# Kernel optimization log

Measured on AMD Instinct MI355X. Metric: run time of the kernel, lower is better.

## Reference

```python
import jax, jax.numpy as jnp
import numpy as np

FEAT = 1024
SUPPORT = 512
N = 4096


def setup_inputs() -> dict:
    key = jax.random.key(0)
    k1, k2, k3, k4, k5, k6 = jax.random.split(key, 6)
    s = 1.0 / np.sqrt(FEAT)
    f = jax.random.normal(k1, (N, FEAT), dtype=jnp.float32)
    G = jax.random.normal(k2, (SUPPORT, FEAT), dtype=jnp.float32)
    # PyTorch LSTMCell params: weight_ih [4*hidden, input], weight_hh [4*hidden, hidden]
    W_ih = jax.random.uniform(k3, (4 * FEAT, 2 * FEAT), minval=-s, maxval=s, dtype=jnp.float32)
    W_hh = jax.random.uniform(k4, (4 * FEAT, FEAT), minval=-s, maxval=s, dtype=jnp.float32)
    b_ih = jax.random.uniform(k5, (4 * FEAT,), minval=-s, maxval=s, dtype=jnp.float32)
    b_hh = jax.random.uniform(k6, (4 * FEAT,), minval=-s, maxval=s, dtype=jnp.float32)
    return {"f": f, "G": G, "W_ih": W_ih, "W_hh": W_hh, "b_ih": b_ih, "b_hh": b_hh, "n_ways": 20}


def _lstm_cell(x, h, c, W_ih, W_hh, b_ih, b_hh):
    # gates ordered i, f, g, o as in torch.nn.LSTMCell
    gates = x @ W_ih.T + b_ih + h @ W_hh.T + b_hh  # [N, 4*FEAT]
    i, fg, g, o = jnp.split(gates, 4, axis=1)
    i = jax.nn.sigmoid(i)
    fg = jax.nn.sigmoid(fg)
    g = jnp.tanh(g)
    o = jax.nn.sigmoid(o)
    c_new = fg * c + i * g
    h_new = o * jnp.tanh(c_new)
    return h_new, c_new


def reference(f, G, W_ih, W_hh, b_ih, b_hh, n_ways):
    h = f
    c = jnp.zeros_like(f)  # c_0 expanded, zeros (non-learned Variable)
    for _ in range(n_ways):
        logit_a = h @ G.T                      # [N, M]
        a = jax.nn.softmax(logit_a, axis=0)    # softmax over dim 0, as in original
        r = a @ G                              # [N, FEAT]
        x = jnp.concatenate((f, r), axis=1)    # [N, 2*FEAT]
        h, c = _lstm_cell(x, h, c, W_ih, W_hh, b_ih, b_hh)
        h = h + f
    return h
```

## Files before the change

### kernel.cpp

```cpp
#include <hip/hip_runtime.h>
#include <math.h>

#define NB    4096
#define FEAT  1024
#define MSUP  512
#define G4    4096
#define NWAYS 20

typedef _Float16 f16;
typedef f16 f16x8 __attribute__((ext_vector_type(8)));
typedef f16 f16x4 __attribute__((ext_vector_type(4)));
typedef float f32x4 __attribute__((ext_vector_type(4)));
typedef unsigned int u32;
#define GLOBAL_AS __attribute__((address_space(1)))
#define LDS_AS    __attribute__((address_space(3)))

__device__ __forceinline__ void load_lds16(const void* g, void* l) {
    __builtin_amdgcn_global_load_lds((const GLOBAL_AS u32*)g, (LDS_AS u32*)l, 16, 0, 0);
}

__device__ __forceinline__ float sigm(float x) { return 1.f / (1.f + __expf(-x)); }

template<int BM, int BN, int WROWS, int WCOLS, bool OUTF16, bool HASBIAS>
__global__ __launch_bounds__(256) void mfma_nt(
    void* __restrict__ Cv, int ldc,
    const f16* __restrict__ A1, int lda1, const f16* __restrict__ B1, int ldb1, int K1,
    const f16* __restrict__ A2, int lda2, const f16* __restrict__ B2, int ldb2, int K2,
    const f16* __restrict__ A3, int lda3, const f16* __restrict__ B3, int ldb3, int K3,
    const float* __restrict__ bias)
{
    constexpr int BK = 32;
    constexpr int WM = BM / WROWS, WN = BN / WCOLS;
    constexpr int FM = WM / 16,   FN = WN / 16;
    __shared__ f16 As[BM][BK];
    __shared__ f16 Bs[BN][BK];
    const int tid  = threadIdx.x;
    const int lane = tid & 63;
    const int wrow = (tid >> 6) % WROWS, wcol = (tid >> 6) / WROWS;
    const int bm = blockIdx.y * BM, bn = blockIdx.x * BN;
    const int lr = lane & 15, lq = lane >> 4;

    f32x4 acc[FM][FN] = {};

    #pragma unroll
    for (int pass = 0; pass < 3; ++pass) {
        const f16* A = pass == 0 ? A1 : (pass == 1 ? A2 : A3);
        const f16* B = pass == 0 ? B1 : (pass == 1 ? B2 : B3);
        const int lda = pass == 0 ? lda1 : (pass == 1 ? lda2 : lda3);
        const int ldb = pass == 0 ? ldb1 : (pass == 1 ? ldb2 : ldb3);
        const int K   = pass == 0 ? K1  : (pass == 1 ? K2  : K3);
        if (!A) break;
        #pragma unroll 1
        for (int k0 = 0; k0 < K; k0 += BK) {
            __syncthreads();
            #pragma unroll
            for (int t = 0; t < (BM * 4) / 256; ++t) {
                int c = t * 256 + tid;
                load_lds16(A + (size_t)(bm + (c >> 2)) * lda + k0 + (c & 3) * 8,
                           &As[0][0] + ((size_t)t * 256 + (tid & 192)) * 8);
            }
            #pragma unroll
            for (int t = 0; t < (BN * 4) / 256; ++t) {
                int c = t * 256 + tid;
                load_lds16(B + (size_t)(bn + (c >> 2)) * ldb + k0 + (c & 3) * 8,
                           &Bs[0][0] + ((size_t)t * 256 + (tid & 192)) * 8);
            }
            __syncthreads();
            f16x8 af[FM], bf[FN];
            #pragma unroll
            for (int i = 0; i < FM; ++i)
                af[i] = *(const f16x8*)&As[wrow * WM + i * 16 + lr][lq * 8];
            #pragma unroll
            for (int j = 0; j < FN; ++j)
                bf[j] = *(const f16x8*)&Bs[wcol * WN + j * 16 + lr][lq * 8];
            #pragma unroll
            for (int i = 0; i < FM; ++i)
                #pragma unroll
                for (int j = 0; j < FN; ++j)
                    acc[i][j] = __builtin_amdgcn_mfma_f32_16x16x32_f16(af[i], bf[j], acc[i][j], 0, 0, 0);
        }
    }

    #pragma unroll
    for (int i = 0; i < FM; ++i) {
        #pragma unroll
        for (int j = 0; j < FN; ++j) {
            const int col  = bn + wcol * WN + j * 16 + lr;
            const int row0 = bm + wrow * WM + i * 16 + lq * 4;
            float badd = HASBIAS ? bias[col] : 0.f;
            #pragma unroll
            for (int r = 0; r < 4; ++r) {
                size_t off = (size_t)(row0 + r) * ldc + col;
                float v = acc[i][j][r] + badd;
                if (OUTF16) ((f16*)Cv)[off] = (f16)v;
                else        ((float*)Cv)[off] = v;
            }
        }
    }
}

__global__ __launch_bounds__(512, 2) void gates_8p(
    const f16* __restrict__ a,
    const f16* __restrict__ h,
    const f16* __restrict__ Wcat,
    const f16* __restrict__ pre,
    const float* __restrict__ fin,
    float* __restrict__ cbuf,
    f16* __restrict__ hh,
    float* __restrict__ hout,
    int first, int writeH)
{
    extern __shared__ f16x8 smem8[];
    f16* smem = (f16*)smem8;
    const int tid  = threadIdx.x;
    const int lane = tid & 63;
    const int wid  = tid >> 6;
    const int wrow = wid >> 2, wcol = wid & 3;
    const int lr = lane & 15, lq = lane >> 4;

    const int bidr = blockIdx.y * 16 + blockIdx.x;
    const int wg   = (bidr & 7) * 32 + (bidr >> 3);
    const int bm = (wg >> 4) * 256;
    const int bn = (wg & 15) * 256;

    f32x4 acc[8][4] = {};

    auto stage = [&](const f16* src, int ld, int rb, int ko, f16* lbase, int l) {
        int c = l * 512 + tid;
        int r = c >> 3;
        int x = (c & 7) ^ (r & 7);
        load_lds16(src + (size_t)(rb + r) * ld + ko + (x << 3),
                   lbase + ((size_t)(l * 512 + (tid & 448))) * 8);
    };
    #define RDF(BUF, RB, KK) \
        (*(const f16x8*)((BUF) + ((size_t)((RB) + lr) << 6) + ((((KK) << 2 | lq) ^ (lr & 7)) << 3)))
    #define BAR()  asm volatile("s_barrier" ::: "memory")
    #define SBAR() __builtin_amdgcn_sched_barrier(0)

    #pragma unroll
    for (int l = 0; l < 4; ++l) {
        stage(Wcat, 2048, bn, 0, smem + 16384, l);
        stage(a,    MSUP, bm, 0, smem,         l);
    }
    asm volatile("s_waitcnt vmcnt(0)" ::: "memory");
    BAR();

    #pragma unroll 1
    for (int t = 0; t < 32; ++t) {
        f16* Ab = smem + (t & 1) * 32768;
        f16* Bb = Ab + 16384;
        f16* An = smem + ((t + 1) & 1) * 32768;
        f16* Bn = An + 16384;
        const int k1 = (t + 1) * 64;
        const f16* As2 = a; int lda2 = MSUP, ko2 = k1;
        if (k1 >= 1024)     { As2 = h; lda2 = FEAT; ko2 = k1 - 1024; }
        else if (k1 >= 512) { ko2 = k1 - 512; }
        const bool st = (t < 31);

        f16x8 af[4][2], bf[2][2], bg[2][2];

        #pragma unroll
        for (int i = 0; i < 4; ++i)
            #pragma unroll
            for (int kk = 0; kk < 2; ++kk)
                af[i][kk] = RDF(Ab, wrow * 128 + i * 16, kk);
        #pragma unroll
        for (int j = 0; j < 2; ++j)
            #pragma unroll
            for (int kk = 0; kk < 2; ++kk)
                bf[j][kk] = RDF(Bb, wcol * 64 + j * 16, kk);
        if (st) {
            stage(Wcat, 2048, bn, k1, Bn, 0);
            stage(Wcat, 2048, bn, k1, Bn, 1);
            stage(Wcat, 2048, bn, k1, Bn, 2);
        }
        BAR(); SBAR();
        __builtin_amdgcn_s_setprio(1);
        #pragma unroll
        for (int kk = 0; kk < 2; ++kk)
            #pragma unroll
            for (int i = 0; i < 4; ++i)
                #pragma unroll
                for (int j = 0; j < 2; ++j)
                    acc[i][j] = __builtin_amdgcn_mfma_f32_16x16x32_f16(af[i][kk], bf[j][kk], acc[i][j], 0, 0, 0);
        __builtin_amdgcn_s_setprio(0);
        BAR();

        #pragma unroll
        for (int j = 0; j < 2; ++j)
            #pragma unroll
            for (int kk = 0; kk < 2; ++kk)
                bg[j][kk] = RDF(Bb, wcol * 64 + (j + 2) * 16, kk);
        if (st) {
            stage(Wcat, 2048, bn, k1, Bn, 3);
            stage(As2, lda2, bm, ko2, An, 0);
            stage(As2, lda2, bm, ko2, An, 2);
        }
        BAR(); SBAR();
        __builtin_amdgcn_s_setprio(1);
        #pragma unroll
        for (int kk = 0; kk < 2; ++kk)
            #pragma unroll
            for (int i = 0; i < 4; ++i)
                #pragma unroll
                for (int j = 0; j < 2; ++j)
                    acc[i][j + 2] = __builtin_amdgcn_mfma_f32_16x16x32_f16(af[i][kk], bg[j][kk], acc[i][j + 2], 0, 0, 0);
        __builtin_amdgcn_s_setprio(0);
        if (st) asm volatile("s_waitcnt vmcnt(6)" ::: "memory");
        else    asm volatile("s_waitcnt vmcnt(0)" ::: "memory");
        BAR();

        #pragma unroll
        for (int i = 0; i < 4; ++i)
            #pragma unroll
            for (int kk = 0; kk < 2; ++kk)
                af[i][kk] = RDF(Ab, wrow * 128 + (i + 4) * 16, kk);
        if (st) {
            stage(As2, lda2, bm, ko2, An, 1);
            stage(As2, lda2, bm, ko2, An, 3);
        }
        BAR(); SBAR();
        __builtin_amdgcn_s_setprio(1);
        #pragma unroll
        for (int kk = 0; kk < 2; ++kk)
            #pragma unroll
            for (int i = 0; i < 4; ++i)
                #pragma unroll
                for (int j = 0; j < 2; ++j)
                    acc[i + 4][j + 2] = __builtin_amdgcn_mfma_f32_16x16x32_f16(af[i][kk], bg[j][kk], acc[i + 4][j + 2], 0, 0, 0);
        __builtin_amdgcn_s_setprio(0);
        BAR();

        #pragma unroll
        for (int j = 0; j < 2; ++j)
            #pragma unroll
            for (int kk = 0; kk < 2; ++kk)
                bf[j][kk] = RDF(Bb, wcol * 64 + j * 16, kk);
        BAR(); SBAR();
        __builtin_amdgcn_s_setprio(1);
        #pragma unroll
        for (int kk = 0; kk < 2; ++kk)
            #pragma unroll
            for (int i = 0; i < 4; ++i)
                #pragma unroll
                for (int j = 0; j < 2; ++j)
                    acc[i + 4][j] = __builtin_amdgcn_mfma_f32_16x16x32_f16(af[i][kk], bf[j][kk], acc[i + 4][j], 0, 0, 0);
        __builtin_amdgcn_s_setprio(0);
        if (st) asm volatile("s_waitcnt vmcnt(2)" ::: "memory");
        BAR();
    }
    #undef RDF

    const int q  = lane & 3;
    const int fk = (lane >> 2) & 3;
    #pragma unroll
    for (int i = 0; i < 8; ++i) {
        #pragma unroll
        for (int j = 0; j < 4; ++j) {
            const int cb   = bn + wcol * 64 + j * 16;
            const int row0 = bm + wrow * 128 + i * 16 + lq * 4;
            float x[4];
            #pragma unroll
            for (int r = 0; r < 4; ++r) x[r] = acc[i][j][r];
            float g4[4];
            #pragma unroll
            for (int k = 0; k < 4; ++k) {
                int srcq = (q + k) & 3;
                int src  = (lane & ~3) | srcq;
                g4[srcq] = __shfl(x[(q - k + 4) & 3], src, 64);
            }
            const int row  = row0 + q;
            const int feat = (cb >> 2) + fk;
            f16x4 p = *(const f16x4*)(pre + (size_t)row * G4 + cb + 4 * fk);
            const float i_ = sigm(g4[0] + (float)p[0]);
            const float f_ = sigm(g4[1] + (float)p[1]);
            const float g_ = tanhf(g4[2] + (float)p[2]);
            const float o_ = sigm(g4[3] + (float)p[3]);
            const size_t cid = ((size_t)(blockIdx.y * gridDim.x + blockIdx.x) * 32
                                + i * 4 + j) * 512 + tid;
            float cold = first ? 0.f : cbuf[cid];
            float cn = i_ * g_ + f_ * cold;
            cbuf[cid] = cn;
            float hn = o_ * tanhf(cn) + fin[(size_t)row * FEAT + feat];
            hh[(size_t)row * FEAT + feat] = (f16)hn;
            if (writeH) hout[(size_t)row * FEAT + feat] = hn;
        }
    }
}

__global__ __launch_bounds__(256) void softmax_rows_kernel(
    const float* __restrict__ X, f16* __restrict__ Y)
{
    const int row = blockIdx.x;
    const float* x = X + (size_t)row * NB;
    f16* y = Y + (size_t)row * NB;
    const int tid = threadIdx.x;
    float v[16];
    float mx = -1e30f;
    #pragma unroll
    for (int i = 0; i < 16; ++i) { v[i] = x[tid + (i << 8)]; mx = fmaxf(mx, v[i]); }
    #pragma unroll
    for (int off = 32; off > 0; off >>= 1) mx = fmaxf(mx, __shfl_down(mx, off));
    __shared__ float sm[4];
    if ((tid & 63) == 0) sm[tid >> 6] = mx;
    __syncthreads();
    mx = fmaxf(fmaxf(sm[0], sm[1]), fmaxf(sm[2], sm[3]));
    float s = 0.f;
    #pragma unroll
    for (int i = 0; i < 16; ++i) { v[i] = __expf(v[i] - mx); s += v[i]; }
    #pragma unroll
    for (int off = 32; off > 0; off >>= 1) s += __shfl_down(s, off);
    __shared__ float ss[4];
    if ((tid & 63) == 0) ss[tid >> 6] = s;
    __syncthreads();
    s = ss[0] + ss[1] + ss[2] + ss[3];
    const float inv = 1.f / s;
    #pragma unroll
    for (int i = 0; i < 16; ++i) y[tid + (i << 8)] = (f16)(v[i] * inv);
}

__global__ __launch_bounds__(256) void transpose_f16_kernel(
    const f16* __restrict__ in, f16* __restrict__ out, int R, int C)
{
    __shared__ f16 t[64][65];
    const int r0 = blockIdx.y * 64, c0 = blockIdx.x * 64;
    const int lr = threadIdx.x & 63, lw = threadIdx.x >> 6;
    #pragma unroll
    for (int i = 0; i < 16; ++i) {
        int rr = lw * 16 + i;
        t[rr][lr] = in[(size_t)(r0 + rr) * C + c0 + lr];
    }
    __syncthreads();
    #pragma unroll
    for (int i = 0; i < 16; ++i) {
        int cc = lw * 16 + i;
        out[(size_t)(c0 + cc) * R + r0 + lr] = t[lr][cc];
    }
}

__global__ __launch_bounds__(256) void cvt_f16_kernel(
    const float* __restrict__ in, f16* __restrict__ out, int n)
{
    int idx = (blockIdx.x * 256 + threadIdx.x) * 4;
    if (idx < n) {
        float4 v = *(const float4*)(in + idx);
        f16x4 o = {(f16)v.x, (f16)v.y, (f16)v.z, (f16)v.w};
        *(f16x4*)(out + idx) = o;
    }
}

__global__ __launch_bounds__(256) void cvt_perm_kernel(
    const float* __restrict__ in, f16* __restrict__ out, int ld_in, int ld_out, int col_off)
{
    int idx = (blockIdx.x * 256 + threadIdx.x) * 4;
    int j = idx / ld_in, k = idx % ld_in;
    int dst = 4 * (j & 1023) + (j >> 10);
    float4 v = *(const float4*)(in + idx);
    f16x4 o = {(f16)v.x, (f16)v.y, (f16)v.z, (f16)v.w};
    *(f16x4*)(out + (size_t)dst * ld_out + col_off + k) = o;
}

__global__ __launch_bounds__(256) void bias_perm_kernel(
    const float* __restrict__ bih, const float* __restrict__ bhh, float* __restrict__ out)
{
    int j = blockIdx.x * 256 + threadIdx.x;
    out[4 * (j & 1023) + (j >> 10)] = bih[j] + bhh[j];
}

__global__ __launch_bounds__(256) void split_wcat_kernel(
    const float* __restrict__ in, f16* __restrict__ out)
{
    int idx = (blockIdx.x * 256 + threadIdx.x) * 4;
    int g = idx >> 9, k = idx & 511;
    float4 v = *(const float4*)(in + idx);
    f16x4 hi = {(f16)v.x, (f16)v.y, (f16)v.z, (f16)v.w};
    f16x4 lo = {(f16)(v.x - (float)hi.x), (f16)(v.y - (float)hi.y),
                (f16)(v.z - (float)hi.z), (f16)(v.w - (float)hi.w)};
    *(f16x4*)(out + (size_t)g * 2048 + k) = hi;
    *(f16x4*)(out + (size_t)g * 2048 + 512 + k) = lo;
}

extern "C" void kernel_launch(void* const* d_in, const int* in_sizes, int n_in,
                              void* d_out, int out_size, void* d_ws, size_t ws_size,
                              hipStream_t stream) {
    const float* f   = (const float*)d_in[0];
    const float* G   = (const float*)d_in[1];
    const float* Wih = (const float*)d_in[2];
    const float* Whh = (const float*)d_in[3];
    const float* bih = (const float*)d_in[4];
    const float* bhh = (const float*)d_in[5];
    float* h = (float*)d_out;

    char* W = (char*)d_ws;
    f16*   pre_h   = (f16*)(W);
    float* aT      = (float*)(W + (size_t)(32 << 20));
    f16*   aTh     = (f16*)(W + (size_t)(40 << 20));
    f16*   a_h     = (f16*)(W + (size_t)(44 << 20));
    float* cbuf    = (float*)(W + (size_t)(48 << 20));
    f16*   h0      = (f16*)(W + (size_t)(64 << 20));
    f16*   hA      = (f16*)(W + (size_t)(72 << 20));
    f16*   hB      = (f16*)(W + (size_t)(80 << 20));
    f16*   Wih_h   = (f16*)(W + (size_t)(88 << 20));
    f16*   Wcat    = (f16*)(W + (size_t)(104 << 20));
    float* Wr32    = (float*)(W + (size_t)(120 << 20));
    f16*   G_h     = (f16*)(W + (size_t)(128 << 20));
    float* bias_p  = (float*)(W + (size_t)(129 << 20));

    const f16* NF = nullptr;
    const dim3 blk(256);

    hipFuncSetAttribute((const void*)gates_8p,
                        hipFuncAttributeMaxDynamicSharedMemorySize, 131072);

    cvt_f16_kernel<<<(NB * FEAT) / 1024, blk, 0, stream>>>(f, h0, NB * FEAT);
    cvt_perm_kernel<<<(G4 * 2 * FEAT) / 1024, blk, 0, stream>>>(Wih, Wih_h, 2 * FEAT, 2 * FEAT, 0);
    cvt_perm_kernel<<<(G4 * FEAT) / 1024, blk, 0, stream>>>(Whh, Wcat, FEAT, 2048, 1024);
    cvt_f16_kernel<<<(MSUP * FEAT) / 1024, blk, 0, stream>>>(G, G_h, MSUP * FEAT);
    bias_perm_kernel<<<G4 / 256, blk, 0, stream>>>(bih, bhh, bias_p);

    mfma_nt<128, 128, 2, 2, true, true><<<dim3(G4 / 128, NB / 128), blk, 0, stream>>>(
        pre_h, G4,
        h0, FEAT, Wih_h, 2 * FEAT, FEAT,
        NF, 0, NF, 0, 0, NF, 0, NF, 0, 0,
        bias_p);

    mfma_nt<128, 128, 2, 2, false, false><<<dim3(MSUP / 128, G4 / 128), blk, 0, stream>>>(
        Wr32, MSUP,
        Wih_h + FEAT, 2 * FEAT, G_h, FEAT, FEAT,
        NF, 0, NF, 0, 0, NF, 0, NF, 0, 0,
        nullptr);
    split_wcat_kernel<<<(G4 * MSUP) / 1024, blk, 0, stream>>>(Wr32, Wcat);

    const f16* hcur = h0;
    for (int it = 0; it < NWAYS; ++it) {
        mfma_nt<64, 64, 2, 2, false, false><<<dim3(NB / 64, MSUP / 64), blk, 0, stream>>>(
            aT, NB,
            G_h, FEAT, hcur, FEAT, FEAT,
            NF, 0, NF, 0, 0, NF, 0, NF, 0, 0,
            nullptr);

        softmax_rows_kernel<<<MSUP, blk, 0, stream>>>(aT, aTh);
        transpose_f16_kernel<<<dim3(NB / 64, MSUP / 64), blk, 0, stream>>>(aTh, a_h, MSUP, NB);

        f16* hnext = (it & 1) ? hB : hA;
        gates_8p<<<dim3(G4 / 256, NB / 256), 512, 131072, stream>>>(
            a_h, hcur, Wcat, pre_h, f, cbuf, hnext, h, it == 0, it == NWAYS - 1);
        hcur = hnext;
    }
}
```

Baseline: 2.436 ms.

## Restructure fused LSTM GEMM main loop with inline-asm LDS reads and prefetch

Rewrites the 256x256 fused LSTM gate GEMM main loop to issue LDS reads through inline-asm ds_read_b128 with precomputed swizzled base addresses and immediate offsets. The loop is unrolled by two so double-buffer addresses are constants. All eight global-to-LDS stages for the next tile are issued at once after a vmcnt wait, and the A/B fragments for the next tile are prefetched during the last MFMA block of the current tile. Fine-grained lgkmcnt waits replace full barriers between sub-blocks. This aims to cut address arithmetic and LDS-read latency stalls, at the cost of more registers and hand-managed waitcnt correctness.

```diff
diff --git a/kernel.cpp b/kernel.cpp
--- a/kernel.cpp
+++ b/kernel.cpp
@@ -20,6 +20,14 @@
 }
 
 __device__ __forceinline__ float sigm(float x) { return 1.f / (1.f + __expf(-x)); }
+
+#define RD(dst, base, OFF) \
+    asm volatile("ds_read_b128 %0, %1 offset:" OFF : "=v"(dst) : "v"(base))
+
+__device__ __forceinline__ f32x4 mfma16(f32x4 a, f32x4 b, f32x4 c) {
+    return __builtin_amdgcn_mfma_f32_16x16x32_f16(
+        __builtin_bit_cast(f16x8, a), __builtin_bit_cast(f16x8, b), c, 0, 0, 0);
+}
 
 template<int BM, int BN, int WROWS, int WCOLS, bool OUTF16, bool HASBIAS>
 __global__ __launch_bounds__(256) void mfma_nt(
@@ -125,56 +133,75 @@
 
     f32x4 acc[8][4] = {};
 
-    auto stage = [&](const f16* src, int ld, int rb, int ko, f16* lbase, int l) {
-        int c = l * 512 + tid;
-        int r = c >> 3;
-        int x = (c & 7) ^ (r & 7);
-        load_lds16(src + (size_t)(rb + r) * ld + ko + (x << 3),
-                   lbase + ((size_t)(l * 512 + (tid & 448))) * 8);
+    const int rr8 = tid >> 3;
+    const int xx8 = ((tid & 7) ^ (rr8 & 7)) << 3;
+    const int plA = rr8 * MSUP + xx8;
+    const int plH = rr8 * FEAT + xx8;
+    const int plW = rr8 * 2048 + xx8;
+    const int ldst = (tid & 448) * 8;
+
+    auto stageW = [&](int ko, f16* lbase, int l) {
+        load_lds16(Wcat + (size_t)(bn + l * 64) * 2048 + ko + plW,
+                   lbase + l * 4096 + ldst);
     };
-    #define RDF(BUF, RB, KK) \
-        (*(const f16x8*)((BUF) + ((size_t)((RB) + lr) << 6) + ((((KK) << 2 | lq) ^ (lr & 7)) << 3)))
-    #define BAR()  asm volatile("s_barrier" ::: "memory")
-    #define SBAR() __builtin_amdgcn_sched_barrier(0)
-
-    #pragma unroll
-    for (int l = 0; l < 4; ++l) {
-        stage(Wcat, 2048, bn, 0, smem + 16384, l);
-        stage(a,    MSUP, bm, 0, smem,         l);
-    }
-    asm volatile("s_waitcnt vmcnt(0)" ::: "memory");
+    auto stageA = [&](const f16* src, int ld, int pl, int ko, f16* lbase, int l) {
+        load_lds16(src + (size_t)(bm + l * 64) * ld + ko + pl,
+                   lbase + l * 4096 + ldst);
+    };
+
+    const u32 sbase = (u32)(size_t)(void*)smem;
+    const u32 rowA  = (u32)(wrow * 128 + lr) << 7;
+    const u32 rowB  = 32768u + ((u32)(wcol * 64 + lr) << 7);
+    const u32 sz0   = (u32)((lq ^ (lr & 7)) << 4);
+    const u32 sz1   = (u32)(((4 | lq) ^ (lr & 7)) << 4);
+    const u32 A0k0 = sbase + rowA + sz0,          A0k1 = sbase + rowA + sz1;
+    const u32 B0k0 = sbase + rowB + sz0,          B0k1 = sbase + rowB + sz1;
+    const u32 A1k0 = A0k0 + 65536u,               A1k1 = A0k1 + 65536u;
+    const u32 B1k0 = B0k0 + 65536u,               B1k1 = B0k1 + 65536u;
+
+    #define BAR()    asm volatile("s_barrier" ::: "memory")
+    #define LGKM(N)  asm volatile("s_waitcnt lgkmcnt(" #N ")" ::: "memory")
+    #define VMC(N)   asm volatile("s_waitcnt vmcnt(" #N ")" ::: "memory")
+    #define SBAR()   __builtin_amdgcn_sched_barrier(0)
+
+    f32x4 aL[4][2], aH[4][2], b0[2][2], b1[2][2];
+
+    stageW(0, smem + 16384, 0); stageW(0, smem + 16384, 1);
+    stageW(0, smem + 16384, 2); stageW(0, smem + 16384, 3);
+    stageA(a, MSUP, plA, 0, smem, 0); stageA(a, MSUP, plA, 0, smem, 2);
+    stageA(a, MSUP, plA, 0, smem, 1); stageA(a, MSUP, plA, 0, smem, 3);
+    VMC(2);
     BAR();
-
-    #pragma unroll 1
-    for (int t = 0; t < 32; ++t) {
-        f16* Ab = smem + (t & 1) * 32768;
-        f16* Bb = Ab + 16384;
-        f16* An = smem + ((t + 1) & 1) * 32768;
-        f16* Bn = An + 16384;
-        const int k1 = (t + 1) * 64;
-        const f16* As2 = a; int lda2 = MSUP, ko2 = k1;
-        if (k1 >= 1024)     { As2 = h; lda2 = FEAT; ko2 = k1 - 1024; }
+    RD(aL[0][0], A0k0, "0");    RD(aL[1][0], A0k0, "2048");
+    RD(aL[2][0], A0k0, "4096"); RD(aL[3][0], A0k0, "6144");
+    RD(aL[0][1], A0k1, "0");    RD(aL[1][1], A0k1, "2048");
+    RD(aL[2][1], A0k1, "4096"); RD(aL[3][1], A0k1, "6144");
+    RD(b0[0][0], B0k0, "0");    RD(b0[1][0], B0k0, "2048");
+    RD(b0[0][1], B0k1, "0");    RD(b0[1][1], B0k1, "2048");
+
+    auto tile_body = [&](int tt,
+                         u32 cA0, u32 cA1, u32 cB0, u32 cB1,
+                         u32 nA0, u32 nA1, u32 nB0, u32 nB1,
+                         f16* An_, f16* Bn_) {
+        const bool st = (tt < 31);
+        const int k1 = (tt + 1) * 64;
+        const f16* As2 = a; int lda2 = MSUP, pl2 = plA, ko2 = k1;
+        if (k1 >= 1024)     { As2 = h; lda2 = FEAT; pl2 = plH; ko2 = k1 - 1024; }
         else if (k1 >= 512) { ko2 = k1 - 512; }
-        const bool st = (t < 31);
-
-        f16x8 af[4][2], bf[2][2], bg[2][2];
-
-        #pragma unroll
-        for (int i = 0; i < 4; ++i)
-            #pragma unroll
-            for (int kk = 0; kk < 2; ++kk)
-                af[i][kk] = RDF(Ab, wrow * 128 + i * 16, kk);
-        #pragma unroll
-        for (int j = 0; j < 2; ++j)
-            #pragma unroll
-            for (int kk = 0; kk < 2; ++kk)
-                bf[j][kk] = RDF(Bb, wcol * 64 + j * 16, kk);
+
+        VMC(0);
+        BAR();
         if (st) {
-            stage(Wcat, 2048, bn, k1, Bn, 0);
-            stage(Wcat, 2048, bn, k1, Bn, 1);
-            stage(Wcat, 2048, bn, k1, Bn, 2);
+            stageW(k1, Bn_, 0); stageW(k1, Bn_, 1);
+            stageW(k1, Bn_, 2); stageW(k1, Bn_, 3);
+            stageA(As2, lda2, pl2, ko2, An_, 0); stageA(As2, lda2, pl2, ko2, An_, 2);
+            stageA(As2, lda2, pl2, ko2, An_, 1); stageA(As2, lda2, pl2, ko2, An_, 3);
         }
-        BAR(); SBAR();
+        RD(aH[0][0], cA0, "8192");  RD(aH[1][0], cA0, "10240");
+        RD(aH[2][0], cA0, "12288"); RD(aH[3][0], cA0, "14336");
+        RD(aH[0][1], cA1, "8192");  RD(aH[1][1], cA1, "10240");
+        RD(aH[2][1], cA1, "12288"); RD(aH[3][1], cA1, "14336");
+        LGKM(8); SBAR();
         __builtin_amdgcn_s_setprio(1);
         #pragma unroll
         for (int kk = 0; kk < 2; ++kk)
@@ -182,21 +209,13 @@
             for (int i = 0; i < 4; ++i)
                 #pragma unroll
                 for (int j = 0; j < 2; ++j)
-                    acc[i][j] = __builtin_amdgcn_mfma_f32_16x16x32_f16(af[i][kk], bf[j][kk], acc[i][j], 0, 0, 0);
+                    acc[i][j] = mfma16(aL[i][kk], b0[j][kk], acc[i][j]);
         __builtin_amdgcn_s_setprio(0);
+
         BAR();
-
-        #pragma unroll
-        for (int j = 0; j < 2; ++j)
-            #pragma unroll
-            for (int kk = 0; kk < 2; ++kk)
-                bg[j][kk] = RDF(Bb, wcol * 64 + (j + 2) * 16, kk);
-        if (st) {
-            stage(Wcat, 2048, bn, k1, Bn, 3);
-            stage(As2, lda2, bm, ko2, An, 0);
-            stage(As2, lda2, bm, ko2, An, 2);
-        }
-        BAR(); SBAR();
+        RD(b1[0][0], cB0, "4096"); RD(b1[1][0], cB0, "6144");
+        RD(b1[0][1], cB1, "4096"); RD(b1[1][1], cB1, "6144");
+        LGKM(4); SBAR();
         __builtin_amdgcn_s_setprio(1);
         #pragma unroll
         for (int kk = 0; kk < 2; ++kk)
@@ -204,22 +223,11 @@
             for (int i = 0; i < 4; ++i)
                 #pragma unroll
                 for (int j = 0; j < 2; ++j)
-                    acc[i][j + 2] = __builtin_amdgcn_mfma_f32_16x16x32_f16(af[i][kk], bg[j][kk], acc[i][j + 2], 0, 0, 0);
+                    acc[i + 4][j] = mfma16(aH[i][kk], b0[j][kk], acc[i + 4][j]);
         __builtin_amdgcn_s_setprio(0);
-        if (st) asm volatile("s_waitcnt vmcnt(6)" ::: "memory");
-        else    asm volatile("s_waitcnt vmcnt(0)" ::: "memory");
+
         BAR();
-
-        #pragma unroll
-        for (int i = 0; i < 4; ++i)
-            #pragma unroll
-            for (int kk = 0; kk < 2; ++kk)
-                af[i][kk] = RDF(Ab, wrow * 128 + (i + 4) * 16, kk);
-        if (st) {
-            stage(As2, lda2, bm, ko2, An, 1);
-            stage(As2, lda2, bm, ko2, An, 3);
-        }
-        BAR(); SBAR();
+        LGKM(0); SBAR();
         __builtin_amdgcn_s_setprio(1);
         #pragma unroll
         for (int kk = 0; kk < 2; ++kk)
@@ -227,16 +235,20 @@
             for (int i = 0; i < 4; ++i)
                 #pragma unroll
                 for (int j = 0; j < 2; ++j)
-                    acc[i + 4][j + 2] = __builtin_amdgcn_mfma_f32_16x16x32_f16(af[i][kk], bg[j][kk], acc[i + 4][j + 2], 0, 0, 0);
+                    acc[i][j + 2] = mfma16(aL[i][kk], b1[j][kk], acc[i][j + 2]);
         __builtin_amdgcn_s_setprio(0);
+
+        if (st) { VMC(2); } else { VMC(0); }
         BAR();
-
-        #pragma unroll
-        for (int j = 0; j < 2; ++j)
-            #pragma unroll
-            for (int kk = 0; kk < 2; ++kk)
-                bf[j][kk] = RDF(Bb, wcol * 64 + j * 16, kk);
-        BAR(); SBAR();
+        if (st) {
+            RD(aL[0][0], nA0, "0");    RD(aL[1][0], nA0, "2048");
+            RD(aL[2][0], nA0, "4096"); RD(aL[3][0], nA0, "6144");
+            RD(aL[0][1], nA1, "0");    RD(aL[1][1], nA1, "2048");
+            RD(aL[2][1], nA1, "4096"); RD(aL[3][1], nA1, "6144");
+            RD(b0[0][0], nB0, "0");    RD(b0[1][0], nB0, "2048");
+            RD(b0[0][1], nB1, "0");    RD(b0[1][1], nB1, "2048");
+        }
+        SBAR();
         __builtin_amdgcn_s_setprio(1);
         #pragma unroll
         for (int kk = 0; kk < 2; ++kk)
@@ -244,12 +256,17 @@
             for (int i = 0; i < 4; ++i)
                 #pragma unroll
                 for (int j = 0; j < 2; ++j)
-                    acc[i + 4][j] = __builtin_amdgcn_mfma_f32_16x16x32_f16(af[i][kk], bf[j][kk], acc[i + 4][j], 0, 0, 0);
+                    acc[i + 4][j + 2] = mfma16(aH[i][kk], b1[j][kk], acc[i + 4][j + 2]);
         __builtin_amdgcn_s_setprio(0);
-        if (st) asm volatile("s_waitcnt vmcnt(2)" ::: "memory");
-        BAR();
-    }
-    #undef RDF
+    };
+
+    #pragma unroll 1
+    for (int t2 = 0; t2 < 32; t2 += 2) {
+        tile_body(t2,     A0k0, A0k1, B0k0, B0k1,  A1k0, A1k1, B1k0, B1k1,
+                  smem + 32768, smem + 49152);
+        tile_body(t2 + 1, A1k0, A1k1, B1k0, B1k1,  A0k0, A0k1, B0k0, B0k1,
+                  smem, smem + 16384);
+    }
 
     const int q  = lane & 3;
     const int fk = (lane >> 2) & 3;
@@ -286,6 +303,10 @@
             if (writeH) hout[(size_t)row * FEAT + feat] = hn;
         }
     }
+    #undef BAR
+    #undef LGKM
+    #undef VMC
+    #undef SBAR
 }
 
 __global__ __launch_bounds__(256) void softmax_rows_kernel(
```

New measurement: 3.089 ms. 26.8% more time.
